# Performance work log

Measured on AMD Instinct MI355X. Metric: run time of the kernel, lower is better.

The kernel has to match this reference:

```python
import jax, jax.numpy as jnp
import numpy as np


def _global_softmax(h):
    # Faithful to soft(): exp over ALL elements, divide by total sum (flattened).
    m = jnp.max(h)  # global max for numerical stability
    e = jnp.exp(h - m)
    return e / jnp.sum(e)


def setup_inputs() -> dict:
    key = jax.random.key(0)
    ks = jax.random.split(key, 7)
    B = 262144
    return {
        "x": jax.random.normal(ks[0], (B, 256), dtype=jnp.float32),
        "wz1": jax.random.normal(ks[1], (256, 64), dtype=jnp.float32) * 0.05,
        "b1": jax.random.normal(ks[2], (1, 64), dtype=jnp.float32),
        "wz2": jax.random.normal(ks[3], (64, 16), dtype=jnp.float32) * 0.1,
        "b2": jax.random.normal(ks[4], (1, 16), dtype=jnp.float32),
        "wz3": jax.random.normal(ks[5], (16, 4), dtype=jnp.float32) * 0.2,
        "b3": jax.random.normal(ks[6], (1, 4), dtype=jnp.float32),
    }


def reference(x, wz1, b1, wz2, b2, wz3, b3):
    h = jax.nn.relu(x @ wz1 + b1)          # [B,64]
    h = jnp.tanh(h @ wz2 + b2)             # [B,16]
    h = h @ wz3 + b3                       # [B,4]
    return _global_softmax(h)              # normalized over all B*4 elements
```

## Files before the change

kernel.cpp:

```cpp
#include <hip/hip_runtime.h>


typedef _Float16 half8 __attribute__((ext_vector_type(8)));
typedef _Float16 half4 __attribute__((ext_vector_type(4)));
typedef float f32x4 __attribute__((ext_vector_type(4)));

#define GRID 256
#define TPB  512
#define TROWS 64

#define XS  264
#define WS  264
#define H1S 72
#define W2S 72

#define SCALE_IN 256.0f
#define SCALE_W  2048.0f
#define INV_SC   (1.0f/524288.0f)

#define OFF_XH  0
#define OFF_XL  (OFF_XH + TROWS*XS*2)
#define OFF_W1H (OFF_XL + TROWS*XS*2)
#define OFF_W1L (OFF_W1H + 64*WS*2)
#define OFF_H1H (OFF_W1L + 64*WS*2)
#define OFF_H1L (OFF_H1H + TROWS*H1S*2)
#define OFF_W2H (OFF_H1L + TROWS*H1S*2)
#define OFF_W2L (OFF_W2H + 16*W2S*2)
#define OFF_SUM (OFF_W2L + 16*W2S*2)
#define SMEM_BYTES (OFF_SUM + 64*4)

extern __shared__ char smem_raw[];

#define MFMA16(a,b,c) __builtin_amdgcn_mfma_f32_16x16x32_f16((a),(b),(c),0,0,0)

__device__ __forceinline__ void lds_barrier() {
    asm volatile("s_waitcnt lgkmcnt(0)\ns_barrier" ::: "memory");
}

__global__ __launch_bounds__(TPB, 2) void fused_mlp(
    const float* __restrict__ x,
    const float* __restrict__ wz1, const float* __restrict__ b1,
    const float* __restrict__ wz2, const float* __restrict__ b2,
    const float* __restrict__ wz3, const float* __restrict__ b3,
    float* __restrict__ Eout, float* __restrict__ block_sums,
    int ntiles)
{
    _Float16* xh  = (_Float16*)(smem_raw + OFF_XH);
    _Float16* xl  = (_Float16*)(smem_raw + OFF_XL);
    _Float16* w1h = (_Float16*)(smem_raw + OFF_W1H);
    _Float16* w1l = (_Float16*)(smem_raw + OFF_W1L);
    _Float16* h1h = (_Float16*)(smem_raw + OFF_H1H);
    _Float16* h1l = (_Float16*)(smem_raw + OFF_H1L);
    _Float16* w2h = (_Float16*)(smem_raw + OFF_W2H);
    _Float16* w2l = (_Float16*)(smem_raw + OFF_W2L);
    float* sums   = (float*)(smem_raw + OFF_SUM);

    const int tid  = threadIdx.x;
    const int lane = tid & 63;
    const int wid  = __builtin_amdgcn_readfirstlane(tid >> 6);
    const int l15  = lane & 15;
    const int g8   = (lane >> 4) * 8;

    const size_t blk_row0 = (size_t)blockIdx.x * ntiles * TROWS;

    float4 xv[8];
    {
        const float4* xg = (const float4*)(x + blk_row0 * 256);
        #pragma unroll
        for (int c = 0; c < 8; ++c) xv[c] = xg[c * TPB + tid];
    }

    {
        const float4* wg = (const float4*)wz1;
        #pragma unroll
        for (int c = 0; c < 8; ++c) {
            const int q = c * TPB + tid;
            const float4 v = wg[q];
            const int k = q >> 4, n0 = (q & 15) * 4;
            const float vv[4] = {v.x, v.y, v.z, v.w};
            #pragma unroll
            for (int i = 0; i < 4; ++i) {
                const float s = vv[i] * SCALE_W;
                const _Float16 h = (_Float16)s;
                w1h[(n0 + i) * WS + k] = h;
                w1l[(n0 + i) * WS + k] = (_Float16)(s - (float)h);
            }
        }
        if (tid < 256) {
            const float4 v = ((const float4*)wz2)[tid];
            const int k = tid >> 2, c0 = (tid & 3) * 4;
            const float vv[4] = {v.x, v.y, v.z, v.w};
            #pragma unroll
            for (int i = 0; i < 4; ++i) {
                const float s = vv[i] * SCALE_W;
                const _Float16 h = (_Float16)s;
                w2h[(c0 + i) * W2S + k] = h;
                w2l[(c0 + i) * W2S + k] = (_Float16)(s - (float)h);
            }
        }
    }

    const int rt  = wid >> 1;
    const int ntp = wid & 1;
    const int col0 = (2 * ntp) * 16 + l15;
    const int col1 = (2 * ntp + 1) * 16 + l15;
    const float b1v0 = b1[col0], b1v1 = b1[col1];
    float b2v[4], w3v[4][4];
    #pragma unroll
    for (int i = 0; i < 4; ++i) {
        const int c2 = (lane >> 4) * 4 + i;
        b2v[i] = b2[c2];
        #pragma unroll
        for (int c3 = 0; c3 < 4; ++c3) w3v[i][c3] = wz3[c2 * 4 + c3];
    }
    const float b3v[4] = {b3[0], b3[1], b3[2], b3[3]};

    lds_barrier();

    half8 Bh[8][2], Bl[8][2];
    #pragma unroll
    for (int kt = 0; kt < 8; ++kt) {
        Bh[kt][0] = *(const half8*)(w1h + col0 * WS + kt * 32 + g8);
        Bh[kt][1] = *(const half8*)(w1h + col1 * WS + kt * 32 + g8);
        Bl[kt][0] = *(const half8*)(w1l + col0 * WS + kt * 32 + g8);
        Bl[kt][1] = *(const half8*)(w1l + col1 * WS + kt * 32 + g8);
    }
    half8 A2h[2], A2l[2];
    #pragma unroll
    for (int kt = 0; kt < 2; ++kt) {
        A2h[kt] = *(const half8*)(w2h + l15 * W2S + kt * 32 + g8);
        A2l[kt] = *(const half8*)(w2l + l15 * W2S + kt * 32 + g8);
    }

    float local_sum = 0.f;

    for (int t = 0; t < ntiles; ++t) {
        #pragma unroll
        for (int c = 0; c < 8; ++c) {
            const float vv[4] = {xv[c].x, xv[c].y, xv[c].z, xv[c].w};
            half4 hh, hl;
            #pragma unroll
            for (int i = 0; i < 4; ++i) {
                const float s = vv[i] * SCALE_IN;
                const _Float16 h = (_Float16)s;
                hh[i] = h;
                hl[i] = (_Float16)(s - (float)h);
            }
            const int row = c * 8 + wid;
            *(half4*)(xh + row * XS + lane * 4) = hh;
            *(half4*)(xl + row * XS + lane * 4) = hl;
        }
        if (t + 1 < ntiles) {
            const float4* xg2 =
                (const float4*)(x + (blk_row0 + (size_t)(t + 1) * TROWS) * 256);
            #pragma unroll
            for (int c = 0; c < 8; ++c) xv[c] = xg2[c * TPB + tid];
        }
        lds_barrier();

        f32x4 acc0 = {0.f, 0.f, 0.f, 0.f}, acc1 = {0.f, 0.f, 0.f, 0.f};
        {
            const _Float16* xh_p = xh + (rt * 16 + l15) * XS;
            const _Float16* xl_p = xl + (rt * 16 + l15) * XS;
            #pragma unroll
            for (int kt = 0; kt < 8; ++kt) {
                const int ko = kt * 32 + g8;
                const half8 ah = *(const half8*)(xh_p + ko);
                const half8 al = *(const half8*)(xl_p + ko);
                acc0 = MFMA16(ah, Bh[kt][0], acc0);
                acc1 = MFMA16(ah, Bh[kt][1], acc1);
                acc0 = MFMA16(al, Bh[kt][0], acc0);
                acc1 = MFMA16(al, Bh[kt][1], acc1);
                acc0 = MFMA16(ah, Bl[kt][0], acc0);
                acc1 = MFMA16(ah, Bl[kt][1], acc1);
            }
        }
        #pragma unroll
        for (int i = 0; i < 4; ++i) {
            const int r = rt * 16 + (lane >> 4) * 4 + i;
            const float h0 = fmaxf(fmaf(acc0[i], INV_SC, b1v0), 0.f);
            const float h1f = fmaxf(fmaf(acc1[i], INV_SC, b1v1), 0.f);
            const float s0 = h0 * SCALE_IN;
            const _Float16 h0h = (_Float16)s0;
            h1h[r * H1S + col0] = h0h;
            h1l[r * H1S + col0] = (_Float16)(s0 - (float)h0h);
            const float s1 = h1f * SCALE_IN;
            const _Float16 h1hh = (_Float16)s1;
            h1h[r * H1S + col1] = h1hh;
            h1l[r * H1S + col1] = (_Float16)(s1 - (float)h1hh);
        }
        lds_barrier();

        if (wid < 4) {
            f32x4 a2 = {0.f, 0.f, 0.f, 0.f};
            const _Float16* hh_p = h1h + (wid * 16 + l15) * H1S;
            const _Float16* hl_p = h1l + (wid * 16 + l15) * H1S;
            #pragma unroll
            for (int kt = 0; kt < 2; ++kt) {
                const int ko = kt * 32 + g8;
                const half8 bh = *(const half8*)(hh_p + ko);
                const half8 bl = *(const half8*)(hl_p + ko);
                a2 = MFMA16(A2h[kt], bh, a2);
                a2 = MFMA16(A2l[kt], bh, a2);
                a2 = MFMA16(A2h[kt], bl, a2);
            }
            float p0 = 0.f, p1 = 0.f, p2 = 0.f, p3 = 0.f;
            #pragma unroll
            for (int i = 0; i < 4; ++i) {
                const float h2 = tanhf(fmaf(a2[i], INV_SC, b2v[i]));
                p0 = fmaf(h2, w3v[i][0], p0);
                p1 = fmaf(h2, w3v[i][1], p1);
                p2 = fmaf(h2, w3v[i][2], p2);
                p3 = fmaf(h2, w3v[i][3], p3);
            }
            p0 += __shfl_xor(p0, 16, 64); p0 += __shfl_xor(p0, 32, 64);
            p1 += __shfl_xor(p1, 16, 64); p1 += __shfl_xor(p1, 32, 64);
            p2 += __shfl_xor(p2, 16, 64); p2 += __shfl_xor(p2, 32, 64);
            p3 += __shfl_xor(p3, 16, 64); p3 += __shfl_xor(p3, 32, 64);
            if (lane < 16) {
                const float e0 = expf(p0 + b3v[0]);
                const float e1 = expf(p1 + b3v[1]);
                const float e2 = expf(p2 + b3v[2]);
                const float e3 = expf(p3 + b3v[3]);
                const size_t row = blk_row0 + (size_t)t * TROWS + wid * 16 + lane;
                float4 ev; ev.x = e0; ev.y = e1; ev.z = e2; ev.w = e3;
                *(float4*)(Eout + row * 4) = ev;
                local_sum += (e0 + e1) + (e2 + e3);
            }
        }
    }

    #pragma unroll
    for (int off = 32; off > 0; off >>= 1)
        local_sum += __shfl_down(local_sum, off, 64);
    if (lane == 0) sums[wid] = local_sum;
    lds_barrier();
    if (tid == 0) {
        float s = 0.f;
        #pragma unroll
        for (int w = 0; w < 8; ++w) s += sums[w];
        block_sums[blockIdx.x] = s;
    }
}

__global__ __launch_bounds__(256) void scale_kernel(
    float* __restrict__ out, const float* __restrict__ block_sums)
{
    __shared__ float red[4];
    const int tid = threadIdx.x;
    float s = block_sums[tid];
    #pragma unroll
    for (int off = 32; off > 0; off >>= 1) s += __shfl_down(s, off, 64);
    if ((tid & 63) == 0) red[tid >> 6] = s;
    __syncthreads();
    const float inv = 1.0f / ((red[0] + red[1]) + (red[2] + red[3]));
    const int idx = blockIdx.x * 256 + tid;
    float4* o4 = (float4*)out;
    float4 v = o4[idx];
    v.x *= inv; v.y *= inv; v.z *= inv; v.w *= inv;
    o4[idx] = v;
}

extern "C" void kernel_launch(void* const* d_in, const int* in_sizes, int n_in,
                              void* d_out, int out_size, void* d_ws, size_t ws_size,
                              hipStream_t stream) {
    (void)n_in; (void)ws_size;
    const float* x   = (const float*)d_in[0];
    const float* wz1 = (const float*)d_in[1];
    const float* b1  = (const float*)d_in[2];
    const float* wz2 = (const float*)d_in[3];
    const float* b2  = (const float*)d_in[4];
    const float* wz3 = (const float*)d_in[5];
    const float* b3  = (const float*)d_in[6];
    float* out = (float*)d_out;

    float* block_sums = (float*)d_ws;

    const int B = in_sizes[0] / 256;
    const int ntiles = B / (GRID * TROWS);

    hipFuncSetAttribute((const void*)fused_mlp,
                        hipFuncAttributeMaxDynamicSharedMemorySize, SMEM_BYTES);

    fused_mlp<<<GRID, TPB, SMEM_BYTES, stream>>>(
        x, wz1, b1, wz2, b2, wz3, b3, out, block_sums, ntiles);

    const int n4 = out_size / 4;
    scale_kernel<<<n4 / 256, 256, 0, stream>>>(out, block_sums);
}
```

Measured before the change: 57.34 us.

## Halve block size and tile rows, load weight fragments directly from global

Blocks shrink from 512 to 256 threads and the grid doubles to 512, with 32-row tiles instead of 64. The LDS staging of the hi/lo split W1 and W2 matrices is removed: each lane now gathers its own weight fragment elements from global memory and splits them in registers. This cuts LDS use per block and drops a barrier, so more blocks can be resident per CU. The cost is strided, uncoalesced global weight loads per lane at kernel start, and the scale kernel now sums 512 block partials.

```diff
diff --git a/kernel.cpp b/kernel.cpp
--- a/kernel.cpp
+++ b/kernel.cpp
@@ -5,14 +5,12 @@
 typedef _Float16 half4 __attribute__((ext_vector_type(4)));
 typedef float f32x4 __attribute__((ext_vector_type(4)));
 
-#define GRID 256
-#define TPB  512
-#define TROWS 64
+#define GRID 512
+#define TPB  256
+#define TROWS 32
 
 #define XS  264
-#define WS  264
 #define H1S 72
-#define W2S 72
 
 #define SCALE_IN 256.0f
 #define SCALE_W  2048.0f
@@ -20,14 +18,10 @@
 
 #define OFF_XH  0
 #define OFF_XL  (OFF_XH + TROWS*XS*2)
-#define OFF_W1H (OFF_XL + TROWS*XS*2)
-#define OFF_W1L (OFF_W1H + 64*WS*2)
-#define OFF_H1H (OFF_W1L + 64*WS*2)
+#define OFF_H1H (OFF_XL + TROWS*XS*2)
 #define OFF_H1L (OFF_H1H + TROWS*H1S*2)
-#define OFF_W2H (OFF_H1L + TROWS*H1S*2)
-#define OFF_W2L (OFF_W2H + 16*W2S*2)
-#define OFF_SUM (OFF_W2L + 16*W2S*2)
-#define SMEM_BYTES (OFF_SUM + 64*4)
+#define OFF_SUM (OFF_H1L + TROWS*H1S*2)
+#define SMEM_BYTES (OFF_SUM + 4*4)
 
 extern __shared__ char smem_raw[];
 
@@ -35,6 +29,17 @@
 
 __device__ __forceinline__ void lds_barrier() {
     asm volatile("s_waitcnt lgkmcnt(0)\ns_barrier" ::: "memory");
+}
+
+__device__ __forceinline__ void split8(const float* v, float scale,
+                                       half8& h, half8& l) {
+    #pragma unroll
+    for (int j = 0; j < 8; ++j) {
+        const float s = v[j] * scale;
+        const _Float16 hi = (_Float16)s;
+        h[j] = hi;
+        l[j] = (_Float16)(s - (float)hi);
+    }
 }
 
 __global__ __launch_bounds__(TPB, 2) void fused_mlp(
@@ -47,19 +52,16 @@
 {
     _Float16* xh  = (_Float16*)(smem_raw + OFF_XH);
     _Float16* xl  = (_Float16*)(smem_raw + OFF_XL);
-    _Float16* w1h = (_Float16*)(smem_raw + OFF_W1H);
-    _Float16* w1l = (_Float16*)(smem_raw + OFF_W1L);
     _Float16* h1h = (_Float16*)(smem_raw + OFF_H1H);
     _Float16* h1l = (_Float16*)(smem_raw + OFF_H1L);
-    _Float16* w2h = (_Float16*)(smem_raw + OFF_W2H);
-    _Float16* w2l = (_Float16*)(smem_raw + OFF_W2L);
     float* sums   = (float*)(smem_raw + OFF_SUM);
 
     const int tid  = threadIdx.x;
     const int lane = tid & 63;
     const int wid  = __builtin_amdgcn_readfirstlane(tid >> 6);
     const int l15  = lane & 15;
-    const int g8   = (lane >> 4) * 8;
+    const int g4   = lane >> 4;
+    const int g8   = g4 * 8;
 
     const size_t blk_row0 = (size_t)blockIdx.x * ntiles * TROWS;
 
@@ -68,36 +70,6 @@
         const float4* xg = (const float4*)(x + blk_row0 * 256);
         #pragma unroll
         for (int c = 0; c < 8; ++c) xv[c] = xg[c * TPB + tid];
-    }
-
-    {
-        const float4* wg = (const float4*)wz1;
-        #pragma unroll
-        for (int c = 0; c < 8; ++c) {
-            const int q = c * TPB + tid;
-            const float4 v = wg[q];
-            const int k = q >> 4, n0 = (q & 15) * 4;
-            const float vv[4] = {v.x, v.y, v.z, v.w};
-            #pragma unroll
-            for (int i = 0; i < 4; ++i) {
-                const float s = vv[i] * SCALE_W;
-                const _Float16 h = (_Float16)s;
-                w1h[(n0 + i) * WS + k] = h;
-                w1l[(n0 + i) * WS + k] = (_Float16)(s - (float)h);
-            }
-        }
-        if (tid < 256) {
-            const float4 v = ((const float4*)wz2)[tid];
-            const int k = tid >> 2, c0 = (tid & 3) * 4;
-            const float vv[4] = {v.x, v.y, v.z, v.w};
-            #pragma unroll
-            for (int i = 0; i < 4; ++i) {
-                const float s = vv[i] * SCALE_W;
-                const _Float16 h = (_Float16)s;
-                w2h[(c0 + i) * W2S + k] = h;
-                w2l[(c0 + i) * W2S + k] = (_Float16)(s - (float)h);
-            }
-        }
     }
 
     const int rt  = wid >> 1;
@@ -108,28 +80,33 @@
     float b2v[4], w3v[4][4];
     #pragma unroll
     for (int i = 0; i < 4; ++i) {
-        const int c2 = (lane >> 4) * 4 + i;
+        const int c2 = g4 * 4 + i;
         b2v[i] = b2[c2];
         #pragma unroll
         for (int c3 = 0; c3 < 4; ++c3) w3v[i][c3] = wz3[c2 * 4 + c3];
     }
     const float b3v[4] = {b3[0], b3[1], b3[2], b3[3]};
 
-    lds_barrier();
-
     half8 Bh[8][2], Bl[8][2];
     #pragma unroll
     for (int kt = 0; kt < 8; ++kt) {
-        Bh[kt][0] = *(const half8*)(w1h + col0 * WS + kt * 32 + g8);
-        Bh[kt][1] = *(const half8*)(w1h + col1 * WS + kt * 32 + g8);
-        Bl[kt][0] = *(const half8*)(w1l + col0 * WS + kt * 32 + g8);
-        Bl[kt][1] = *(const half8*)(w1l + col1 * WS + kt * 32 + g8);
+        float t0[8], t1[8];
+        #pragma unroll
+        for (int j = 0; j < 8; ++j) {
+            const int k = kt * 32 + g8 + j;
+            t0[j] = wz1[k * 64 + col0];
+            t1[j] = wz1[k * 64 + col1];
+        }
+        split8(t0, SCALE_W, Bh[kt][0], Bl[kt][0]);
+        split8(t1, SCALE_W, Bh[kt][1], Bl[kt][1]);
     }
     half8 A2h[2], A2l[2];
     #pragma unroll
     for (int kt = 0; kt < 2; ++kt) {
-        A2h[kt] = *(const half8*)(w2h + l15 * W2S + kt * 32 + g8);
-        A2l[kt] = *(const half8*)(w2l + l15 * W2S + kt * 32 + g8);
+        float tmp[8];
+        #pragma unroll
+        for (int j = 0; j < 8; ++j) tmp[j] = wz2[(kt * 32 + g8 + j) * 16 + l15];
+        split8(tmp, SCALE_W, A2h[kt], A2l[kt]);
     }
 
     float local_sum = 0.f;
@@ -146,7 +123,7 @@
                 hh[i] = h;
                 hl[i] = (_Float16)(s - (float)h);
             }
-            const int row = c * 8 + wid;
+            const int row = c * 4 + wid;
             *(half4*)(xh + row * XS + lane * 4) = hh;
             *(half4*)(xl + row * XS + lane * 4) = hl;
         }
@@ -177,7 +154,7 @@
         }
         #pragma unroll
         for (int i = 0; i < 4; ++i) {
-            const int r = rt * 16 + (lane >> 4) * 4 + i;
+            const int r = rt * 16 + g4 * 4 + i;
             const float h0 = fmaxf(fmaf(acc0[i], INV_SC, b1v0), 0.f);
             const float h1f = fmaxf(fmaf(acc1[i], INV_SC, b1v1), 0.f);
             const float s0 = h0 * SCALE_IN;
@@ -191,7 +168,7 @@
         }
         lds_barrier();
 
-        if (wid < 4) {
+        if (wid < 2) {
             f32x4 a2 = {0.f, 0.f, 0.f, 0.f};
             const _Float16* hh_p = h1h + (wid * 16 + l15) * H1S;
             const _Float16* hl_p = h1l + (wid * 16 + l15) * H1S;
@@ -235,12 +212,8 @@
         local_sum += __shfl_down(local_sum, off, 64);
     if (lane == 0) sums[wid] = local_sum;
     lds_barrier();
-    if (tid == 0) {
-        float s = 0.f;
-        #pragma unroll
-        for (int w = 0; w < 8; ++w) s += sums[w];
-        block_sums[blockIdx.x] = s;
-    }
+    if (tid == 0)
+        block_sums[blockIdx.x] = (sums[0] + sums[1]) + (sums[2] + sums[3]);
 }
 
 __global__ __launch_bounds__(256) void scale_kernel(
@@ -248,7 +221,7 @@
 {
     __shared__ float red[4];
     const int tid = threadIdx.x;
-    float s = block_sums[tid];
+    float s = block_sums[tid] + block_sums[tid + 256];
     #pragma unroll
     for (int off = 32; off > 0; off >>= 1) s += __shfl_down(s, off, 64);
     if ((tid & 63) == 0) red[tid >> 6] = s;
```

Result: slower. 62.45 us (+8.9%).
